# Kernel tuning notes

Measured on AMD Instinct MI355X. Metric: run time of the kernel, lower is better.

The kernel has to match this reference:

```python
import jax, jax.numpy as jnp
import numpy as np

N_HEADS = 16
D_K = 64
DIM = 1024
NEG = -1e12
LN_EPS = 1e-5


def setup_inputs() -> dict:
    key = jax.random.key(0)
    ks = jax.random.split(key, 8)
    B, S, D = 2, 2048, DIM
    H, K = N_HEADS, D_K
    f = lambda k, shp: jax.random.normal(k, shp, dtype=jnp.float32)
    scale = 0.02
    return {
        "input_Q": f(ks[0], (B, S, D)),
        "input_K": f(ks[1], (B, S, D)),
        "input_V": f(ks[2], (B, S, D)),
        "attention_mask": jax.random.randint(ks[3], (B, S), 0, 2, dtype=jnp.int32),
        "W_Q": f(ks[4], (H * K, D)) * scale,  # nn.Linear weight layout [out, in]
        "W_K": f(ks[5], (H * K, D)) * scale,
        "W_V": f(ks[6], (H * K, D)) * scale,
        "W_O": f(ks[7], (D, H * K)) * scale,
        "gamma": jnp.ones((D,), jnp.float32),
        "beta": jnp.zeros((D,), jnp.float32),
    }


def reference(input_Q, input_K, input_V, attention_mask, W_Q, W_K, W_V, W_O, gamma, beta):
    B, S, D = input_Q.shape

    def proj(x, W):  # [B,S,D] @ [HK,D]^T -> [B,H,S,K]
        return (x @ W.T).reshape(B, S, N_HEADS, D_K).transpose(0, 2, 1, 3)

    Q = proj(input_Q, W_Q)
    K = proj(input_K, W_K)
    V = proj(input_V, W_V)

    scores = jnp.einsum('bhqk,bhsk->bhqs', Q, K) / np.float32(np.sqrt(D_K))

    # Faithful reproduction of scores_mask (including its inverted-looking logic):
    # mask = clamp(padding_mask + strict_upper_tri - 1, min=0); scores += (1-mask)*NEG
    am = attention_mask.astype(scores.dtype)[:, None, None, :]          # [B,1,1,S]
    low_tri = jnp.triu(jnp.ones((S, S), scores.dtype), k=1)             # 1 - tril(ones)
    m = jnp.maximum(am + low_tri - 1.0, 0.0)
    scores = scores + (1.0 - m) * NEG

    attn = jax.nn.softmax(scores, axis=-1)
    ctx = jnp.einsum('bhqs,bhsk->bhqk', attn, V)                        # [B,H,S,K]
    ctx = ctx.transpose(0, 2, 1, 3).reshape(B, S, N_HEADS * D_K)

    out = ctx @ W_O.T + input_Q                                         # fc + residual
    mu = jnp.mean(out, axis=-1, keepdims=True)
    var = jnp.var(out, axis=-1, keepdims=True)
    return (out - mu) / jnp.sqrt(var + LN_EPS) * gamma + beta
```

## Files before the change

kernel.cpp:

```cpp
#include <hip/hip_runtime.h>

#define NH    16
#define DK    64
#define DIM   1024
#define BATCH 2
#define SEQ   2048
#define MROWS (BATCH*SEQ)
#define QSCALE 0.18033688011112043f
#define SENT   -44.0f
#define PCONST 5.684341886080802e-14f

typedef unsigned short bfraw;
typedef __attribute__((ext_vector_type(8))) __bf16 bf16x8;
typedef __attribute__((ext_vector_type(8))) unsigned short u16x8;
typedef __attribute__((ext_vector_type(4))) float f32x4;

__device__ __forceinline__ float bf2f(bfraw u) {
    union { unsigned int i; float f; } x; x.i = ((unsigned int)u) << 16; return x.f;
}
__device__ __forceinline__ bfraw f2bf(float f) {
    union { float f; unsigned int i; } x; x.f = f;
    unsigned int r = x.i + 0x7FFFu + ((x.i >> 16) & 1u);
    return (bfraw)(r >> 16);
}
__device__ __forceinline__ bfraw f2bf_trunc(float f) {
    union { float f; unsigned int i; } x; x.f = f;
    return (bfraw)(x.i >> 16);
}
__device__ __forceinline__ float fexp2(float x) {
#if __has_builtin(__builtin_amdgcn_exp2f)
    return __builtin_amdgcn_exp2f(x);
#else
    return exp2f(x);
#endif
}

__device__ __forceinline__ float block_reduce(float val, float* rbuf, int op) {
    const int lane = threadIdx.x & 63, wave = threadIdx.x >> 6;
    #pragma unroll
    for (int off = 32; off; off >>= 1) {
        float o = __shfl_xor(val, off, 64);
        val = op ? (val + o) : fmaxf(val, o);
    }
    if (lane == 0) rbuf[wave] = val;
    __syncthreads();
    float r = op ? (rbuf[0] + rbuf[1] + rbuf[2] + rbuf[3])
                 : fmaxf(fmaxf(rbuf[0], rbuf[1]), fmaxf(rbuf[2], rbuf[3]));
    __syncthreads();
    return r;
}

__global__ __launch_bounds__(256) void cvt_kernel(
        const float* __restrict__ x0, const float* __restrict__ x1, const float* __restrict__ x2,
        const float* __restrict__ w0, const float* __restrict__ w1, const float* __restrict__ w2,
        const float* __restrict__ w3, bfraw* __restrict__ Xb, bfraw* __restrict__ Wb) {
    const int t = blockIdx.y;
    const float* src; bfraw* dst; int n;
    if (t < 3) { src = (t == 0) ? x0 : (t == 1) ? x1 : x2; dst = Xb + t * (MROWS * DIM); n = MROWS * DIM; }
    else { int u = t - 3; src = (u == 0) ? w0 : (u == 1) ? w1 : (u == 2) ? w2 : w3;
           dst = Wb + u * (DIM * DIM); n = DIM * DIM; }
    int idx = (blockIdx.x * 256 + threadIdx.x) * 8;
    if (idx >= n) return;
    f32x4 a = *(const f32x4*)(src + idx);
    f32x4 b = *(const f32x4*)(src + idx + 4);
    u16x8 o;
    #pragma unroll
    for (int j = 0; j < 4; j++) { o[j] = f2bf(a[j]); o[4 + j] = f2bf(b[j]); }
    *(u16x8*)(dst + idx) = o;
}

__device__ __forceinline__ void gemm128(const bfraw* __restrict__ A, const bfraw* __restrict__ B,
                                        int m0, int n0, f32x4 acc[4][4]) {
    __shared__ __align__(16) bfraw As[128 * 64];
    __shared__ __align__(16) bfraw Bs[128 * 64];
    const int tid = threadIdx.x, wave = tid >> 6;
    const int lane = tid & 63, lrow = lane & 15, quad = lane >> 4;
    const int wy = wave >> 1, wx = wave & 1;
    const int swz = lrow & 7;
    const int srow = tid >> 2;
    const int cg0  = (tid & 3) << 1;
    const int gc   = cg0 << 3;
    const int e7   = srow & 7;
    const int o0 = ((cg0 ^ e7) << 3), o1 = (((cg0 | 1) ^ e7) << 3);

    u16x8 ha[4], hb[4];
    const bfraw* pa0 = A + (m0 + srow) * DIM + gc;
    const bfraw* pa1 = A + (m0 + 64 + srow) * DIM + gc;
    const bfraw* pb0 = B + (n0 + srow) * DIM + gc;
    const bfraw* pb1 = B + (n0 + 64 + srow) * DIM + gc;

    #pragma unroll
    for (int i = 0; i < 4; i++)
        #pragma unroll
        for (int j = 0; j < 4; j++) { f32x4 z = {0.f, 0.f, 0.f, 0.f}; acc[i][j] = z; }

    ha[0] = *(const u16x8*)(pa0);     ha[1] = *(const u16x8*)(pa0 + 8);
    ha[2] = *(const u16x8*)(pa1);     ha[3] = *(const u16x8*)(pa1 + 8);
    hb[0] = *(const u16x8*)(pb0);     hb[1] = *(const u16x8*)(pb0 + 8);
    hb[2] = *(const u16x8*)(pb1);     hb[3] = *(const u16x8*)(pb1 + 8);

    for (int k0 = 0; k0 < DIM; k0 += 64) {
        __syncthreads();
        *(u16x8*)&As[srow * 64 + o0]        = ha[0];
        *(u16x8*)&As[srow * 64 + o1]        = ha[1];
        *(u16x8*)&As[(64 + srow) * 64 + o0] = ha[2];
        *(u16x8*)&As[(64 + srow) * 64 + o1] = ha[3];
        *(u16x8*)&Bs[srow * 64 + o0]        = hb[0];
        *(u16x8*)&Bs[srow * 64 + o1]        = hb[1];
        *(u16x8*)&Bs[(64 + srow) * 64 + o0] = hb[2];
        *(u16x8*)&Bs[(64 + srow) * 64 + o1] = hb[3];
        __syncthreads();
        if (k0 + 64 < DIM) {
            const int k1 = k0 + 64;
            ha[0] = *(const u16x8*)(pa0 + k1);     ha[1] = *(const u16x8*)(pa0 + k1 + 8);
            ha[2] = *(const u16x8*)(pa1 + k1);     ha[3] = *(const u16x8*)(pa1 + k1 + 8);
            hb[0] = *(const u16x8*)(pb0 + k1);     hb[1] = *(const u16x8*)(pb0 + k1 + 8);
            hb[2] = *(const u16x8*)(pb1 + k1);     hb[3] = *(const u16x8*)(pb1 + k1 + 8);
        }
        #pragma unroll
        for (int ks = 0; ks < 2; ks++) {
            const int c = (ks << 2) | quad;
            bf16x8 af[4], bfg[4];
            #pragma unroll
            for (int mi = 0; mi < 4; mi++)
                af[mi] = *(const bf16x8*)&As[(wy * 64 + mi * 16 + lrow) * 64 + ((c ^ swz) << 3)];
            #pragma unroll
            for (int ni = 0; ni < 4; ni++)
                bfg[ni] = *(const bf16x8*)&Bs[(wx * 64 + ni * 16 + lrow) * 64 + ((c ^ swz) << 3)];
            #pragma unroll
            for (int mi = 0; mi < 4; mi++)
                #pragma unroll
                for (int ni = 0; ni < 4; ni++)
                    acc[mi][ni] = __builtin_amdgcn_mfma_f32_16x16x32_bf16(af[mi], bfg[ni], acc[mi][ni], 0, 0, 0);
        }
    }
}

__global__ __launch_bounds__(256) void qkv_gemm(
        const bfraw* __restrict__ Xb, const bfraw* __restrict__ Wb,
        bfraw* __restrict__ Qp, bfraw* __restrict__ Kp, bfraw* __restrict__ Vt) {
    const int which = blockIdx.z;
    const bfraw* A = Xb + which * (MROWS * DIM);
    const bfraw* B = Wb + which * (DIM * DIM);
    bfraw* O = (which == 0) ? Qp : (which == 1) ? Kp : Vt;
    const int m0 = blockIdx.x * 128, n0 = blockIdx.y * 128;
    f32x4 acc[4][4];
    gemm128(A, B, m0, n0, acc);
    const int lane = threadIdx.x & 63, wave = threadIdx.x >> 6;
    const int lrow = lane & 15, quad = lane >> 4;
    const int wy = wave >> 1, wx = wave & 1;
    const float scale = (which == 0) ? QSCALE : 1.0f;
    #pragma unroll
    for (int mi = 0; mi < 4; mi++)
        #pragma unroll
        for (int ni = 0; ni < 4; ni++)
            #pragma unroll
            for (int i = 0; i < 4; i++) {
                int m = m0 + wy * 64 + mi * 16 + quad * 4 + i;
                int n = n0 + wx * 64 + ni * 16 + lrow;
                int b = m >> 11, s = m & (SEQ - 1), h = n >> 6, kk = n & (DK - 1);
                bfraw v = f2bf(acc[mi][ni][i] * scale);
                if (which == 2) O[(((b * NH + h) * DK) + kk) * SEQ + s] = v;
                else            O[(((b * NH + h) * SEQ) + s) * DK + kk] = v;
            }
}

__global__ __launch_bounds__(256) void vsum_kernel(const bfraw* __restrict__ Vt,
                                                   float* __restrict__ Scum) {
    __shared__ float Ts[32][65];
    const int bh = blockIdx.x, tid = threadIdx.x;
    const int d = tid & 63, part = tid >> 6;
    const bfraw* vrow = Vt + (bh * DK + d) * SEQ;
    for (int qt = part * 8; qt < part * 8 + 8; qt++) {
        float s = 0.f;
        #pragma unroll
        for (int j = 0; j < 64; j += 8) {
            u16x8 v = *(const u16x8*)(vrow + qt * 64 + j);
            #pragma unroll
            for (int e = 0; e < 8; e++) s += bf2f(v[e]);
        }
        Ts[qt][d] = s;
    }
    __syncthreads();
    if (tid < 64) {
        float run = 0.f;
        for (int qt = 0; qt < 32; qt++) {
            Scum[(bh * 32 + qt) * 64 + tid] = run;
            run += Ts[qt][tid];
        }
    }
}

__global__ __launch_bounds__(256) void attn_flash(
        const bfraw* __restrict__ Qp, const bfraw* __restrict__ Kp, const bfraw* __restrict__ Vt,
        const float* __restrict__ Scum, const int* __restrict__ mask, bfraw* __restrict__ Ctx) {
    __shared__ __align__(16) bfraw Ks[64 * 64];
    __shared__ __align__(16) bfraw Vs[64 * 64];
    __shared__ __align__(16) bfraw Pw[4][16 * 68];
    __shared__ unsigned short Mk[SEQ];
    const int bh = blockIdx.x, yy = blockIdx.y;
    const int gg = yy >> 3, jj = yy & 7;
    const int qt = (gg == 0) ? jj : (gg == 1) ? (31 - jj) : (gg == 2) ? (8 + jj) : (23 - jj);
    const int b = bh >> 4, h = bh & 15;
    const int tid = threadIdx.x, wave = tid >> 6, lane = tid & 63;
    const int lrow = lane & 15, quad = lane >> 4;
    const int baseK = ((b * NH + h) * SEQ) * DK;
    const int baseV = ((b * NH + h) * DK) * SEQ;
    const int qbase = qt * 64 + wave * 16;
    const int diagKt = qt * 64;
    const int ldr = tid >> 2;
    const int cg0 = (tid & 3) << 1;
    const int ldc = cg0 << 3;
    const int e7 = ldr & 7;
    const int cl0 = ((cg0 ^ e7) << 3), cl1 = (((cg0 | 1) ^ e7) << 3);

    for (int i = tid; i < SEQ; i += 256) Mk[i] = (unsigned short)(mask[b * SEQ + i] != 0);

    bf16x8 qf[2];
    qf[0] = *(const bf16x8*)(Qp + baseK + (qbase + lrow) * DK + quad * 8);
    qf[1] = *(const bf16x8*)(Qp + baseK + (qbase + lrow) * DK + 32 + quad * 8);

    f32x4 O[4]; float lsum[4];
    #pragma unroll
    for (int n = 0; n < 4; n++) {
        float base = PCONST * Scum[(bh * 32 + qt) * 64 + n * 16 + lrow];
        #pragma unroll
        for (int i = 0; i < 4; i++) O[n][i] = base;
    }
    #pragma unroll
    for (int i = 0; i < 4; i++) lsum[i] = 0.f;

    __syncthreads();

    for (int kt0 = diagKt; kt0 < SEQ; kt0 += 64) {
        u16x8 k0 = *(const u16x8*)(Kp + baseK + (kt0 + ldr) * DK + ldc);
        u16x8 k1 = *(const u16x8*)(Kp + baseK + (kt0 + ldr) * DK + ldc + 8);
        u16x8 v0 = *(const u16x8*)(Vt + baseV + ldr * SEQ + kt0 + ldc);
        u16x8 v1 = *(const u16x8*)(Vt + baseV + ldr * SEQ + kt0 + ldc + 8);
        __syncthreads();
        *(u16x8*)&Ks[ldr * 64 + cl0] = k0;
        *(u16x8*)&Ks[ldr * 64 + cl1] = k1;
        *(u16x8*)&Vs[ldr * 64 + cl0] = v0;
        *(u16x8*)&Vs[ldr * 64 + cl1] = v1;
        __syncthreads();

        f32x4 S[4];
        #pragma unroll
        for (int n = 0; n < 4; n++) {
            const int s = n * 16 + lrow;
            f32x4 z = {0.f, 0.f, 0.f, 0.f};
            #pragma unroll
            for (int ks = 0; ks < 2; ks++) {
                bf16x8 kb = *(const bf16x8*)&Ks[s * 64 + ((((ks << 2) | quad) ^ (s & 7)) << 3)];
                z = __builtin_amdgcn_mfma_f32_16x16x32_bf16(qf[ks], kb, z, 0, 0, 0);
            }
            S[n] = z;
        }

        float p[4][4];
        if (kt0 == diagKt) {
            #pragma unroll
            for (int n = 0; n < 4; n++) {
                int s = kt0 + n * 16 + lrow;
                bool mk = (Mk[s] != 0);
                #pragma unroll
                for (int i = 0; i < 4; i++) {
                    bool valid = mk && (s > qbase + quad * 4 + i);
                    p[n][i] = fexp2(valid ? S[n][i] : SENT);
                }
            }
        } else {
            #pragma unroll
            for (int n = 0; n < 4; n++) {
                bool mk = (Mk[kt0 + n * 16 + lrow] != 0);
                #pragma unroll
                for (int i = 0; i < 4; i++) p[n][i] = fexp2(mk ? S[n][i] : SENT);
            }
        }

        #pragma unroll
        for (int i = 0; i < 4; i++) lsum[i] += (p[0][i] + p[1][i]) + (p[2][i] + p[3][i]);

        #pragma unroll
        for (int n = 0; n < 4; n++)
            #pragma unroll
            for (int i = 0; i < 4; i++)
                Pw[wave][(quad * 4 + i) * 68 + n * 16 + lrow] = f2bf_trunc(p[n][i]);

        bf16x8 pa0 = *(const bf16x8*)&Pw[wave][lrow * 68 + quad * 8];
        bf16x8 pa1 = *(const bf16x8*)&Pw[wave][lrow * 68 + 32 + quad * 8];
        #pragma unroll
        for (int n = 0; n < 4; n++) {
            const int d = n * 16 + lrow;
            #pragma unroll
            for (int ks = 0; ks < 2; ks++) {
                bf16x8 vb = *(const bf16x8*)&Vs[d * 64 + ((((ks << 2) | quad) ^ (d & 7)) << 3)];
                O[n] = __builtin_amdgcn_mfma_f32_16x16x32_bf16(ks ? pa1 : pa0, vb, O[n], 0, 0, 0);
            }
        }
    }

    float inv[4];
    #pragma unroll
    for (int i = 0; i < 4; i++) {
        float r = lsum[i];
        #pragma unroll
        for (int off = 1; off < 16; off <<= 1) r += __shfl_xor(r, off, 64);
        inv[i] = 1.0f / (r + (float)diagKt * PCONST);
    }
    #pragma unroll
    for (int n = 0; n < 4; n++)
        #pragma unroll
        for (int i = 0; i < 4; i++)
            Ctx[(b * SEQ + qbase + quad * 4 + i) * DIM + h * DK + n * 16 + lrow] = f2bf(O[n][i] * inv[i]);
}

__global__ __launch_bounds__(256) void out_gemm(
        const bfraw* __restrict__ Ctx, const bfraw* __restrict__ WoB, float* __restrict__ C) {
    const int m0 = blockIdx.x * 128, n0 = blockIdx.y * 128;
    f32x4 acc[4][4];
    gemm128(Ctx, WoB, m0, n0, acc);
    const int lane = threadIdx.x & 63, wave = threadIdx.x >> 6;
    const int lrow = lane & 15, quad = lane >> 4;
    const int wy = wave >> 1, wx = wave & 1;
    #pragma unroll
    for (int mi = 0; mi < 4; mi++)
        #pragma unroll
        for (int ni = 0; ni < 4; ni++)
            #pragma unroll
            for (int i = 0; i < 4; i++) {
                int m = m0 + wy * 64 + mi * 16 + quad * 4 + i;
                int n = n0 + wx * 64 + ni * 16 + lrow;
                C[m * DIM + n] = acc[mi][ni][i];
            }
}

__global__ __launch_bounds__(256) void ln_kernel(
        const float* __restrict__ C, const float* __restrict__ Xq,
        const float* __restrict__ gamma, const float* __restrict__ beta,
        float* __restrict__ out) {
    __shared__ float rbuf[4];
    const int m = blockIdx.x, tid = threadIdx.x;
    const float* crow = C + m * DIM;
    const float* xrow = Xq + m * DIM;
    float v[4]; float s = 0.f, s2 = 0.f;
    #pragma unroll
    for (int i = 0; i < 4; i++) {
        int d = tid + (i << 8);
        float x = crow[d] + xrow[d];
        v[i] = x; s += x; s2 += x * x;
    }
    float S  = block_reduce(s,  rbuf, 1);
    float S2 = block_reduce(s2, rbuf, 1);
    float mu  = S * (1.0f / DIM);
    float var = S2 * (1.0f / DIM) - mu * mu;
    float rstd = rsqrtf(var + 1e-5f);
    #pragma unroll
    for (int i = 0; i < 4; i++) {
        int d = tid + (i << 8);
        out[m * DIM + d] = (v[i] - mu) * rstd * gamma[d] + beta[d];
    }
}

extern "C" void kernel_launch(void* const* d_in, const int* in_sizes, int n_in,
                              void* d_out, int out_size, void* d_ws, size_t ws_size,
                              hipStream_t stream) {
    const float* Xq    = (const float*)d_in[0];
    const float* Xk    = (const float*)d_in[1];
    const float* Xv    = (const float*)d_in[2];
    const int*   mask  = (const int*)  d_in[3];
    const float* Wq    = (const float*)d_in[4];
    const float* Wk    = (const float*)d_in[5];
    const float* Wv    = (const float*)d_in[6];
    const float* Wo    = (const float*)d_in[7];
    const float* gamma = (const float*)d_in[8];
    const float* beta  = (const float*)d_in[9];
    float* out = (float*)d_out;

    char* ws = (char*)d_ws;
    bfraw* Xb   = (bfraw*)(ws);
    bfraw* Wb   = (bfraw*)(ws + (24u << 20));
    bfraw* Qp   = (bfraw*)(ws + (32u << 20));
    bfraw* Kp   = (bfraw*)(ws + (40u << 20));
    bfraw* Vt   = (bfraw*)(ws + (48u << 20));
    bfraw* Ctx  = (bfraw*)(ws + (56u << 20));
    float* C    = (float*)(ws);
    float* Scum = (float*)(ws + (16u << 20));

    dim3 blk(256);
    cvt_kernel<<<dim3(MROWS * DIM / (256 * 8), 7), blk, 0, stream>>>(Xq, Xk, Xv, Wq, Wk, Wv, Wo, Xb, Wb);
    qkv_gemm  <<<dim3(MROWS / 128, DIM / 128, 3),  blk, 0, stream>>>(Xb, Wb, Qp, Kp, Vt);
    vsum_kernel<<<dim3(BATCH * NH),                blk, 0, stream>>>(Vt, Scum);
    attn_flash<<<dim3(BATCH * NH, SEQ / 64),       blk, 0, stream>>>(Qp, Kp, Vt, Scum, mask, Ctx);
    out_gemm  <<<dim3(MROWS / 128, DIM / 128),     blk, 0, stream>>>(Ctx, Wb + 3 * (DIM * DIM), C);
    ln_kernel <<<dim3(MROWS),                      blk, 0, stream>>>(C, Xq, gamma, beta, out);
}
```

Measured before the change: 229.3 us.

## Transpose attention MFMAs to keep P in registers and double-buffer K/V tiles

The flash-attention kernel now computes S transposed (K as the A operand, Q as B), so each lane holds probabilities for one query row in the layout the PV MFMA expects. That removes the per-wave shared-memory P round-trip and lets PV use 16x16x16 bf16 MFMAs fed directly from registers. K/V tiles are double-buffered in LDS with the next tile's global loads issued before the barrier, cutting one __syncthreads per iteration and overlapping loads with compute. The trade-offs are twice as many smaller PV MFMAs, more LDS, and a more complex swizzled V read pattern.

```diff
diff --git a/kernel.cpp b/kernel.cpp
--- a/kernel.cpp
+++ b/kernel.cpp
@@ -12,7 +12,10 @@
 
 typedef unsigned short bfraw;
 typedef __attribute__((ext_vector_type(8))) __bf16 bf16x8;
+typedef __attribute__((ext_vector_type(4))) __bf16 bf16x4;
 typedef __attribute__((ext_vector_type(8))) unsigned short u16x8;
+typedef __attribute__((ext_vector_type(4))) unsigned short u16x4;
+typedef __attribute__((ext_vector_type(4))) short s16x4;
 typedef __attribute__((ext_vector_type(4))) float f32x4;
 
 __device__ __forceinline__ float bf2f(bfraw u) {
@@ -32,6 +35,18 @@
     return __builtin_amdgcn_exp2f(x);
 #else
     return exp2f(x);
+#endif
+}
+
+__device__ __forceinline__ f32x4 mfma16(s16x4 a, s16x4 b, f32x4 c) {
+#if __has_builtin(__builtin_amdgcn_mfma_f32_16x16x16_bf16)
+    union { s16x4 s; bf16x4 h; } ua, ub; ua.s = a; ub.s = b;
+    return __builtin_amdgcn_mfma_f32_16x16x16_bf16(ua.h, ub.h, c, 0, 0, 0);
+#elif __has_builtin(__builtin_amdgcn_mfma_f32_16x16x16bf16_1k)
+    return __builtin_amdgcn_mfma_f32_16x16x16bf16_1k(a, b, c, 0, 0, 0);
+#else
+    asm("v_mfma_f32_16x16x16_bf16 %0, %1, %2, %0" : "+v"(c) : "v"(a), "v"(b));
+    return c;
 #endif
 }
 
@@ -194,9 +209,8 @@
 __global__ __launch_bounds__(256) void attn_flash(
         const bfraw* __restrict__ Qp, const bfraw* __restrict__ Kp, const bfraw* __restrict__ Vt,
         const float* __restrict__ Scum, const int* __restrict__ mask, bfraw* __restrict__ Ctx) {
-    __shared__ __align__(16) bfraw Ks[64 * 64];
-    __shared__ __align__(16) bfraw Vs[64 * 64];
-    __shared__ __align__(16) bfraw Pw[4][16 * 68];
+    __shared__ __align__(16) bfraw Ks[2][64 * 64];
+    __shared__ __align__(16) bfraw Vs[2][64 * 64];
     __shared__ unsigned short Mk[SEQ];
     const int bh = blockIdx.x, yy = blockIdx.y;
     const int gg = yy >> 3, jj = yy & 7;
@@ -207,6 +221,7 @@
     const int baseK = ((b * NH + h) * SEQ) * DK;
     const int baseV = ((b * NH + h) * DK) * SEQ;
     const int qbase = qt * 64 + wave * 16;
+    const int q_ln  = qbase + lrow;
     const int diagKt = qt * 64;
     const int ldr = tid >> 2;
     const int cg0 = (tid & 3) << 1;
@@ -220,99 +235,90 @@
     qf[0] = *(const bf16x8*)(Qp + baseK + (qbase + lrow) * DK + quad * 8);
     qf[1] = *(const bf16x8*)(Qp + baseK + (qbase + lrow) * DK + 32 + quad * 8);
 
-    f32x4 O[4]; float lsum[4];
-    #pragma unroll
-    for (int n = 0; n < 4; n++) {
-        float base = PCONST * Scum[(bh * 32 + qt) * 64 + n * 16 + lrow];
-        #pragma unroll
-        for (int i = 0; i < 4; i++) O[n][i] = base;
-    }
-    #pragma unroll
-    for (int i = 0; i < 4; i++) lsum[i] = 0.f;
-
-    __syncthreads();
-
-    for (int kt0 = diagKt; kt0 < SEQ; kt0 += 64) {
-        u16x8 k0 = *(const u16x8*)(Kp + baseK + (kt0 + ldr) * DK + ldc);
-        u16x8 k1 = *(const u16x8*)(Kp + baseK + (kt0 + ldr) * DK + ldc + 8);
-        u16x8 v0 = *(const u16x8*)(Vt + baseV + ldr * SEQ + kt0 + ldc);
-        u16x8 v1 = *(const u16x8*)(Vt + baseV + ldr * SEQ + kt0 + ldc + 8);
+    f32x4 Oa[4];
+    #pragma unroll
+    for (int nd = 0; nd < 4; nd++) {
+        f32x4 sv = *(const f32x4*)&Scum[(bh * 32 + qt) * 64 + nd * 16 + quad * 4];
+        #pragma unroll
+        for (int i = 0; i < 4; i++) Oa[nd][i] = PCONST * sv[i];
+    }
+    float lsum = 0.f;
+
+    const int nt = (SEQ - diagKt) >> 6;
+    int kt0 = diagKt;
+    u16x8 k0 = *(const u16x8*)(Kp + baseK + (kt0 + ldr) * DK + ldc);
+    u16x8 k1 = *(const u16x8*)(Kp + baseK + (kt0 + ldr) * DK + ldc + 8);
+    u16x8 v0 = *(const u16x8*)(Vt + baseV + ldr * SEQ + kt0 + ldc);
+    u16x8 v1 = *(const u16x8*)(Vt + baseV + ldr * SEQ + kt0 + ldc + 8);
+
+    for (int t = 0; t < nt; t++, kt0 += 64) {
+        bfraw* Kb = Ks[t & 1];
+        bfraw* Vb = Vs[t & 1];
+        *(u16x8*)&Kb[ldr * 64 + cl0] = k0;
+        *(u16x8*)&Kb[ldr * 64 + cl1] = k1;
+        *(u16x8*)&Vb[ldr * 64 + cl0] = v0;
+        *(u16x8*)&Vb[ldr * 64 + cl1] = v1;
+        if (t + 1 < nt) {
+            const int kn = kt0 + 64;
+            k0 = *(const u16x8*)(Kp + baseK + (kn + ldr) * DK + ldc);
+            k1 = *(const u16x8*)(Kp + baseK + (kn + ldr) * DK + ldc + 8);
+            v0 = *(const u16x8*)(Vt + baseV + ldr * SEQ + kn + ldc);
+            v1 = *(const u16x8*)(Vt + baseV + ldr * SEQ + kn + ldc + 8);
+        }
         __syncthreads();
-        *(u16x8*)&Ks[ldr * 64 + cl0] = k0;
-        *(u16x8*)&Ks[ldr * 64 + cl1] = k1;
-        *(u16x8*)&Vs[ldr * 64 + cl0] = v0;
-        *(u16x8*)&Vs[ldr * 64 + cl1] = v1;
-        __syncthreads();
-
-        f32x4 S[4];
+
+        s16x4 pb[4];
         #pragma unroll
         for (int n = 0; n < 4; n++) {
-            const int s = n * 16 + lrow;
+            const int srow = n * 16 + lrow;
+            bf16x8 kfa = *(const bf16x8*)&Kb[srow * 64 + ((quad ^ (lrow & 7)) << 3)];
+            bf16x8 kfb = *(const bf16x8*)&Kb[srow * 64 + (((4 | quad) ^ (lrow & 7)) << 3)];
             f32x4 z = {0.f, 0.f, 0.f, 0.f};
-            #pragma unroll
-            for (int ks = 0; ks < 2; ks++) {
-                bf16x8 kb = *(const bf16x8*)&Ks[s * 64 + ((((ks << 2) | quad) ^ (s & 7)) << 3)];
-                z = __builtin_amdgcn_mfma_f32_16x16x32_bf16(qf[ks], kb, z, 0, 0, 0);
-            }
-            S[n] = z;
-        }
-
-        float p[4][4];
-        if (kt0 == diagKt) {
-            #pragma unroll
-            for (int n = 0; n < 4; n++) {
-                int s = kt0 + n * 16 + lrow;
-                bool mk = (Mk[s] != 0);
+            z = __builtin_amdgcn_mfma_f32_16x16x32_bf16(kfa, qf[0], z, 0, 0, 0);
+            z = __builtin_amdgcn_mfma_f32_16x16x32_bf16(kfb, qf[1], z, 0, 0, 0);
+            u16x4 pu;
+            if (t == 0) {
                 #pragma unroll
                 for (int i = 0; i < 4; i++) {
-                    bool valid = mk && (s > qbase + quad * 4 + i);
-                    p[n][i] = fexp2(valid ? S[n][i] : SENT);
+                    int s = kt0 + n * 16 + quad * 4 + i;
+                    bool valid = (Mk[s] != 0) && (s > q_ln);
+                    float p = fexp2(valid ? z[i] : SENT);
+                    lsum += p; pu[i] = f2bf_trunc(p);
+                }
+            } else {
+                #pragma unroll
+                for (int i = 0; i < 4; i++) {
+                    int s = kt0 + n * 16 + quad * 4 + i;
+                    float p = fexp2(Mk[s] ? z[i] : SENT);
+                    lsum += p; pu[i] = f2bf_trunc(p);
                 }
             }
-        } else {
-            #pragma unroll
-            for (int n = 0; n < 4; n++) {
-                bool mk = (Mk[kt0 + n * 16 + lrow] != 0);
-                #pragma unroll
-                for (int i = 0; i < 4; i++) p[n][i] = fexp2(mk ? S[n][i] : SENT);
+            union { u16x4 u; s16x4 s; } cv; cv.u = pu; pb[n] = cv.s;
+        }
+
+        #pragma unroll
+        for (int nd = 0; nd < 4; nd++) {
+            const int d = nd * 16 + lrow;
+            #pragma unroll
+            for (int sc = 0; sc < 4; sc++) {
+                s16x4 vf = *(const s16x4*)&Vb[d * 64
+                    + ((((sc << 1) | (quad >> 1)) ^ (d & 7)) << 3) + ((quad & 1) << 2)];
+                Oa[nd] = mfma16(vf, pb[sc], Oa[nd]);
             }
         }
-
-        #pragma unroll
-        for (int i = 0; i < 4; i++) lsum[i] += (p[0][i] + p[1][i]) + (p[2][i] + p[3][i]);
-
-        #pragma unroll
-        for (int n = 0; n < 4; n++)
-            #pragma unroll
-            for (int i = 0; i < 4; i++)
-                Pw[wave][(quad * 4 + i) * 68 + n * 16 + lrow] = f2bf_trunc(p[n][i]);
-
-        bf16x8 pa0 = *(const bf16x8*)&Pw[wave][lrow * 68 + quad * 8];
-        bf16x8 pa1 = *(const bf16x8*)&Pw[wave][lrow * 68 + 32 + quad * 8];
-        #pragma unroll
-        for (int n = 0; n < 4; n++) {
-            const int d = n * 16 + lrow;
-            #pragma unroll
-            for (int ks = 0; ks < 2; ks++) {
-                bf16x8 vb = *(const bf16x8*)&Vs[d * 64 + ((((ks << 2) | quad) ^ (d & 7)) << 3)];
-                O[n] = __builtin_amdgcn_mfma_f32_16x16x32_bf16(ks ? pa1 : pa0, vb, O[n], 0, 0, 0);
-            }
-        }
-    }
-
-    float inv[4];
-    #pragma unroll
-    for (int i = 0; i < 4; i++) {
-        float r = lsum[i];
-        #pragma unroll
-        for (int off = 1; off < 16; off <<= 1) r += __shfl_xor(r, off, 64);
-        inv[i] = 1.0f / (r + (float)diagKt * PCONST);
-    }
-    #pragma unroll
-    for (int n = 0; n < 4; n++)
-        #pragma unroll
-        for (int i = 0; i < 4; i++)
-            Ctx[(b * SEQ + qbase + quad * 4 + i) * DIM + h * DK + n * 16 + lrow] = f2bf(O[n][i] * inv[i]);
+    }
+
+    float r = lsum;
+    r += __shfl_xor(r, 16, 64);
+    r += __shfl_xor(r, 32, 64);
+    const float inv = 1.0f / (r + (float)diagKt * PCONST);
+    #pragma unroll
+    for (int nd = 0; nd < 4; nd++) {
+        u16x4 o;
+        #pragma unroll
+        for (int i = 0; i < 4; i++) o[i] = f2bf(Oa[nd][i] * inv);
+        *(u16x4*)&Ctx[(b * SEQ + q_ln) * DIM + h * DK + nd * 16 + quad * 4] = o;
+    }
 }
 
 __global__ __launch_bounds__(256) void out_gemm(
```

After: 224.1 us. -2.3%, faster.
